# Kernel optimization log

Measured on AMD Instinct MI355X. Metric: run time of the kernel, lower is better.

## Reference

```python
import jax, jax.numpy as jnp
import numpy as np

EPS = 1e-5

def _layernorm(x, g, b):
    m = jnp.mean(x, axis=-1, keepdims=True)
    v = jnp.mean((x - m) ** 2, axis=-1, keepdims=True)
    return (x - m) * jax.lax.rsqrt(v + EPS) * g + b

def setup_inputs() -> dict:
    key = jax.random.key(0)
    ks = jax.random.split(key, 20)
    B, H, D = 8192, 50, 128
    NUM_USERS, NUM_NEWS, NUM_GNN = 200000, 100000, 80000
    s = 0.05
    user_table = jax.random.normal(ks[0], (NUM_USERS, D), jnp.float32) * s
    news_table = jax.random.normal(ks[1], (NUM_NEWS, D), jnp.float32) * s
    news_table = news_table.at[0].set(0.0)  # padding_idx=0
    inp = {
        "user_idx": jax.random.randint(ks[2], (B,), 0, NUM_USERS, jnp.int64 if jax.config.jax_enable_x64 else jnp.int32),
        "news_idx": jax.random.randint(ks[3], (B,), 0, NUM_NEWS, jnp.int32),
        "history": jax.random.randint(ks[4], (B, H), 0, NUM_NEWS, jnp.int32),
        "gnn_embeddings": jax.random.normal(ks[5], (NUM_GNN, D), jnp.float32) * s,
        "user_table": user_table,
        "news_table": news_table,
        "fusion_w": jax.random.normal(ks[6], (2 * D, D), jnp.float32) * s,
        "fusion_b": jnp.zeros((D,), jnp.float32),
        "ln_g": jnp.ones((D,), jnp.float32),
        "ln_b": jnp.zeros((D,), jnp.float32),
        "attn1_w": jax.random.normal(ks[7], (D, D // 2), jnp.float32) * s,
        "attn1_b": jnp.zeros((D // 2,), jnp.float32),
        "attn2_w": jax.random.normal(ks[8], (D // 2, 1), jnp.float32) * s,
        "attn2_b": jnp.zeros((1,), jnp.float32),
        "ut_w": jax.random.normal(ks[9], (D, D), jnp.float32) * s,
        "ut_b": jnp.zeros((D,), jnp.float32),
        "nt_w": jax.random.normal(ks[10], (D, D), jnp.float32) * s,
        "nt_b": jnp.zeros((D,), jnp.float32),
    }
    return inp

def reference(user_idx, news_idx, history, gnn_embeddings, user_table, news_table,
              fusion_w, fusion_b, ln_g, ln_b, attn1_w, attn1_b, attn2_w, attn2_b,
              ut_w, ut_b, nt_w, nt_b):
    num_gnn = gnn_embeddings.shape[0]

    def gather_gnn(idx):
        # masked gather: zeros where idx >= num_gnn
        valid = idx < num_gnn
        g = gnn_embeddings[jnp.clip(idx, 0, num_gnn - 1)]
        return jnp.where(valid[..., None], g, 0.0)

    def fusion(x):  # Linear(2D->D) + LayerNorm + ReLU (dropout=identity in eval)
        return jax.nn.relu(_layernorm(x @ fusion_w + fusion_b, ln_g, ln_b))

    # ---- user representation ----
    user_emb = user_table[user_idx]                       # (B, D)
    hist_id_emb = news_table[history]                     # (B, H, D)
    hist_gnn_emb = gather_gnn(history)                    # (B, H, D)
    hist_emb = fusion(jnp.concatenate([hist_id_emb, hist_gnn_emb], axis=-1))  # (B, H, D)
    mask = (history != 0)[..., None]                      # (B, H, 1)
    scores_h = jnp.tanh(hist_emb @ attn1_w + attn1_b) @ attn2_w + attn2_b      # (B, H, 1)
    scores_h = jnp.where(mask, scores_h, -1e9)
    attn = jax.nn.softmax(scores_h, axis=1)
    hist_repr = jnp.sum(hist_emb * attn, axis=1)          # (B, D)
    user_repr = jax.nn.relu((user_emb + hist_repr) @ ut_w + ut_b)

    # ---- news representation ----
    id_emb = news_table[news_idx]                         # (B, D)
    gnn_emb = gather_gnn(news_idx)
    fused = fusion(jnp.concatenate([id_emb, gnn_emb], axis=-1))
    news_repr = jax.nn.relu(fused @ nt_w + nt_b)

    return jax.nn.sigmoid(jnp.sum(user_repr * news_repr, axis=1))  # (B,)
```

## Files before the change

### kernel.cpp

```cpp
#include <hip/hip_runtime.h>
#include <math.h>

typedef __attribute__((ext_vector_type(8))) short bf16x8;
typedef __attribute__((ext_vector_type(4))) float f32x4;

#define TPB 256
#define HROWS 50
#define DDIM 128

static __device__ __forceinline__ unsigned short bf16_rne(float x) {
  union { float f; unsigned u; } v; v.f = x;
  return (unsigned short)((v.u + 0x7fffu + ((v.u >> 16) & 1u)) >> 16);
}
static __device__ __forceinline__ float bf16f(unsigned short h) {
  union { float f; unsigned u; } v; v.u = ((unsigned)h) << 16; return v.f;
}
static __device__ __forceinline__ void cvt_hilo(const float4 a, const float4 b,
                                                bf16x8& hi, bf16x8& lo) {
  unsigned short h;
  h = bf16_rne(a.x); hi[0] = (short)h; lo[0] = (short)bf16_rne(a.x - bf16f(h));
  h = bf16_rne(a.y); hi[1] = (short)h; lo[1] = (short)bf16_rne(a.y - bf16f(h));
  h = bf16_rne(a.z); hi[2] = (short)h; lo[2] = (short)bf16_rne(a.z - bf16f(h));
  h = bf16_rne(a.w); hi[3] = (short)h; lo[3] = (short)bf16_rne(a.w - bf16f(h));
  h = bf16_rne(b.x); hi[4] = (short)h; lo[4] = (short)bf16_rne(b.x - bf16f(h));
  h = bf16_rne(b.y); hi[5] = (short)h; lo[5] = (short)bf16_rne(b.y - bf16f(h));
  h = bf16_rne(b.z); hi[6] = (short)h; lo[6] = (short)bf16_rne(b.z - bf16f(h));
  h = bf16_rne(b.w); hi[7] = (short)h; lo[7] = (short)bf16_rne(b.w - bf16f(h));
}

#define WS_FWT_LO 32768
#define WS_A1T_HI 65536
#define WS_A1T_LO 73728

__global__ void prep_w(const float* __restrict__ fw, const float* __restrict__ a1w,
                       unsigned short* __restrict__ ws) {
  const int t = threadIdx.x, j = blockIdx.x;
  if (j < 128) {
    float x = fw[(size_t)t * 128 + j];
    unsigned short hi = bf16_rne(x);
    unsigned short lo = bf16_rne(x - bf16f(hi));
    ws[j * 256 + t] = hi;
    ws[WS_FWT_LO + j * 256 + t] = lo;
  } else if (t < 128) {
    int jj = j - 128;
    float x = a1w[(size_t)t * 64 + jj];
    unsigned short hi = bf16_rne(x);
    unsigned short lo = bf16_rne(x - bf16f(hi));
    ws[WS_A1T_HI + jj * 128 + t] = hi;
    ws[WS_A1T_LO + jj * 128 + t] = lo;
  }
}

__global__ __launch_bounds__(TPB, 3)
void gnnrec_mfma(const int* __restrict__ user_idx,
                 const int* __restrict__ news_idx,
                 const int* __restrict__ history,
                 const float* __restrict__ gnn, int NGNN,
                 const float* __restrict__ user_table,
                 const float* __restrict__ news_table,
                 const float* __restrict__ fusion_b,
                 const float* __restrict__ ln_g,
                 const float* __restrict__ ln_b,
                 const float* __restrict__ attn1_b,
                 const float* __restrict__ attn2_w,
                 const float* __restrict__ attn2_b,
                 const float* __restrict__ ut_w,
                 const float* __restrict__ ut_b,
                 const float* __restrict__ nt_w,
                 const float* __restrict__ nt_b,
                 const unsigned short* __restrict__ ws,
                 float* __restrict__ out)
{
  __shared__ short WtH[128][40];
  __shared__ short WtL[128][40];
  __shared__ float hist_s[51][132];
  __shared__ float scratch[1024 + 384];
  __shared__ int   idx_s[64];
  __shared__ float score_s[HROWS];

  const int b    = blockIdx.x;
  const int t    = threadIdx.x;
  const int lane = t & 63;
  const int w    = t >> 6;
  const int c15  = lane & 15;
  const int g    = lane >> 4;

  if (t < HROWS)        idx_s[t] = history[b * HROWS + t];
  else if (t == HROWS)  idx_s[t] = news_idx[b];
  else if (t < 64)      idx_s[t] = 0;
  const int uidx = user_idx[b];
  __syncthreads();

  const int arow = 16 * w + c15;
  const int aidx = idx_s[arow];
  const float* news_row = news_table + (size_t)aidx * DDIM;
  const bool   gnn_ok   = aidx < NGNN;
  const float* gnn_row  = gnn + (size_t)(gnn_ok ? aidx : 0) * DDIM;

  f32x4 acc[8];
#pragma unroll
  for (int ct = 0; ct < 8; ++ct) acc[ct] = (f32x4){0.f, 0.f, 0.f, 0.f};

  const int sc = t >> 1, ss = (t & 1) * 16;

  for (int kb = 0; kb < 8; ++kb) {
    {
      const unsigned short* ph = ws + sc * 256 + kb * 32 + ss;
      const unsigned short* pl = ph + WS_FWT_LO;
      bf16x8 h0 = *(const bf16x8*)(ph);
      bf16x8 h1 = *(const bf16x8*)(ph + 8);
      bf16x8 l0 = *(const bf16x8*)(pl);
      bf16x8 l1 = *(const bf16x8*)(pl + 8);
      *(bf16x8*)&WtH[sc][ss]     = h0;
      *(bf16x8*)&WtH[sc][ss + 8] = h1;
      *(bf16x8*)&WtL[sc][ss]     = l0;
      *(bf16x8*)&WtL[sc][ss + 8] = l1;
    }
    float4 x0 = make_float4(0.f, 0.f, 0.f, 0.f);
    float4 x1 = make_float4(0.f, 0.f, 0.f, 0.f);
    if (kb < 4) {
      const float* p = news_row + kb * 32 + g * 8;
      x0 = *(const float4*)(p);
      x1 = *(const float4*)(p + 4);
    } else if (gnn_ok) {
      const float* p = gnn_row + (kb - 4) * 32 + g * 8;
      x0 = *(const float4*)(p);
      x1 = *(const float4*)(p + 4);
    }
    bf16x8 aH, aL;
    cvt_hilo(x0, x1, aH, aL);
    __syncthreads();

#pragma unroll
    for (int ct = 0; ct < 8; ++ct) {
      bf16x8 bH = *(const bf16x8*)&WtH[16 * ct + c15][g * 8];
      bf16x8 bL = *(const bf16x8*)&WtL[16 * ct + c15][g * 8];
      acc[ct] = __builtin_amdgcn_mfma_f32_16x16x32_bf16(aH, bH, acc[ct], 0, 0, 0);
      acc[ct] = __builtin_amdgcn_mfma_f32_16x16x32_bf16(aH, bL, acc[ct], 0, 0, 0);
      acc[ct] = __builtin_amdgcn_mfma_f32_16x16x32_bf16(aL, bH, acc[ct], 0, 0, 0);
    }
    __syncthreads();
  }

  {
    float fbv[8], lgv[8], lbv[8];
#pragma unroll
    for (int ct = 0; ct < 8; ++ct) {
      fbv[ct] = fusion_b[16 * ct + c15];
      lgv[ct] = ln_g[16 * ct + c15];
      lbv[ct] = ln_b[16 * ct + c15];
    }
#pragma unroll
    for (int reg = 0; reg < 4; ++reg) {
      float y[8];
      float s = 0.f, sq = 0.f;
#pragma unroll
      for (int ct = 0; ct < 8; ++ct) {
        y[ct] = acc[ct][reg] + fbv[ct];
        s += y[ct];
        sq += y[ct] * y[ct];
      }
#pragma unroll
      for (int off = 1; off <= 8; off <<= 1) {
        s  += __shfl_xor(s,  off);
        sq += __shfl_xor(sq, off);
      }
      float mean = s * (1.f / 128.f);
      float var  = sq * (1.f / 128.f) - mean * mean;
      float inv  = 1.f / sqrtf(var + 1e-5f);
      int row = 16 * w + 4 * g + reg;
      if (row < 51) {
#pragma unroll
        for (int ct = 0; ct < 8; ++ct) {
          float r = fmaxf((y[ct] - mean) * inv * lgv[ct] + lbv[ct], 0.f);
          hist_s[row][16 * ct + c15] = r;
        }
      }
    }
  }
  __syncthreads();

  const unsigned short* a1T_hi = ws + WS_A1T_HI;
  const unsigned short* a1T_lo = ws + WS_A1T_LO;
  const int hrow = (16 * w + c15) < 51 ? (16 * w + c15) : 50;

  f32x4 acc2[4];
#pragma unroll
  for (int ct = 0; ct < 4; ++ct) acc2[ct] = (f32x4){0.f, 0.f, 0.f, 0.f};

#pragma unroll
  for (int ks = 0; ks < 4; ++ks) {
    float4 h0 = *(const float4*)&hist_s[hrow][ks * 32 + g * 8];
    float4 h1 = *(const float4*)&hist_s[hrow][ks * 32 + g * 8 + 4];
    bf16x8 aH, aL;
    cvt_hilo(h0, h1, aH, aL);
#pragma unroll
    for (int ct = 0; ct < 4; ++ct) {
      const int col = 16 * ct + c15;
      bf16x8 bH = *(const bf16x8*)(a1T_hi + col * 128 + ks * 32 + g * 8);
      bf16x8 bL = *(const bf16x8*)(a1T_lo + col * 128 + ks * 32 + g * 8);
      acc2[ct] = __builtin_amdgcn_mfma_f32_16x16x32_bf16(aH, bH, acc2[ct], 0, 0, 0);
      acc2[ct] = __builtin_amdgcn_mfma_f32_16x16x32_bf16(aH, bL, acc2[ct], 0, 0, 0);
      acc2[ct] = __builtin_amdgcn_mfma_f32_16x16x32_bf16(aL, bH, acc2[ct], 0, 0, 0);
    }
  }

  {
    float a1bv[4], a2wv[4];
#pragma unroll
    for (int ct = 0; ct < 4; ++ct) {
      a1bv[ct] = attn1_b[16 * ct + c15];
      a2wv[ct] = attn2_w[16 * ct + c15];
    }
    const float a2b = attn2_b[0];
#pragma unroll
    for (int reg = 0; reg < 4; ++reg) {
      float p = 0.f;
#pragma unroll
      for (int ct = 0; ct < 4; ++ct)
        p += tanhf(acc2[ct][reg] + a1bv[ct]) * a2wv[ct];
#pragma unroll
      for (int off = 1; off <= 8; off <<= 1) p += __shfl_xor(p, off);
      int row = 16 * w + 4 * g + reg;
      if (row < HROWS && c15 == 0)
        score_s[row] = (idx_s[row] != 0) ? (p + a2b) : -1e9f;
    }
  }
  __syncthreads();

  float mx = -3.0e38f;
  for (int r = 0; r < HROWS; ++r) mx = fmaxf(mx, score_s[r]);
  __syncthreads();
  if (t < HROWS) score_s[t] = __expf(score_s[t] - mx);
  __syncthreads();
  float denom = 0.f;
  for (int r = 0; r < HROWS; ++r) denom += score_s[r];
  const float invd = 1.f / denom;

  float* red = scratch;
  {
    int g8 = t >> 5, j4 = (t & 31) * 4;
    float p0 = 0.f, p1 = 0.f, p2 = 0.f, p3 = 0.f;
    for (int r = g8; r < HROWS; r += 8) {
      float wr = score_s[r] * invd;
      float4 hv = *(const float4*)&hist_s[r][j4];
      p0 = fmaf(wr, hv.x, p0);
      p1 = fmaf(wr, hv.y, p1);
      p2 = fmaf(wr, hv.z, p2);
      p3 = fmaf(wr, hv.w, p3);
    }
    *(float4*)&red[g8 * 128 + j4] = make_float4(p0, p1, p2, p3);
  }
  __syncthreads();

  float* u_s  = scratch + 1024;
  float* ur_s = scratch + 1152;
  float* nr_s = scratch + 1280;
  if (t < 128) {
    float hr = 0.f;
#pragma unroll
    for (int q = 0; q < 8; ++q) hr += red[q * 128 + t];
    u_s[t] = user_table[(size_t)uidx * DDIM + t] + hr;
  }
  __syncthreads();

  {
    int path = t >> 7, j = t & 127;
    const float* Wm  = path ? nt_w : ut_w;
    const float* bm  = path ? nt_b : ut_b;
    const float* src = path ? &hist_s[50][0] : u_s;
    float a = 0.f;
#pragma unroll 8
    for (int k4 = 0; k4 < 32; ++k4) {
      float4 sv = *(const float4*)&src[k4 * 4];
      a = fmaf(sv.x, Wm[(size_t)(k4 * 4 + 0) * 128 + j], a);
      a = fmaf(sv.y, Wm[(size_t)(k4 * 4 + 1) * 128 + j], a);
      a = fmaf(sv.z, Wm[(size_t)(k4 * 4 + 2) * 128 + j], a);
      a = fmaf(sv.w, Wm[(size_t)(k4 * 4 + 3) * 128 + j], a);
    }
    a = fmaxf(a + bm[j], 0.f);
    (path ? nr_s : ur_s)[j] = a;
  }
  __syncthreads();

  if (t < 64) {
    float p = ur_s[t] * nr_s[t] + ur_s[t + 64] * nr_s[t + 64];
    p += __shfl_xor(p, 1);
    p += __shfl_xor(p, 2);
    p += __shfl_xor(p, 4);
    p += __shfl_xor(p, 8);
    p += __shfl_xor(p, 16);
    p += __shfl_xor(p, 32);
    if (t == 0) out[b] = 1.f / (1.f + __expf(-p));
  }
}

extern "C" void kernel_launch(void* const* d_in, const int* in_sizes, int n_in,
                              void* d_out, int out_size, void* d_ws, size_t ws_size,
                              hipStream_t stream) {
  const int*   user_idx   = (const int*)d_in[0];
  const int*   news_idx   = (const int*)d_in[1];
  const int*   history    = (const int*)d_in[2];
  const float* gnn        = (const float*)d_in[3];
  const float* user_table = (const float*)d_in[4];
  const float* news_table = (const float*)d_in[5];
  const float* fusion_w   = (const float*)d_in[6];
  const float* fusion_b   = (const float*)d_in[7];
  const float* ln_g       = (const float*)d_in[8];
  const float* ln_b       = (const float*)d_in[9];
  const float* attn1_w    = (const float*)d_in[10];
  const float* attn1_b    = (const float*)d_in[11];
  const float* attn2_w    = (const float*)d_in[12];
  const float* attn2_b    = (const float*)d_in[13];
  const float* ut_w       = (const float*)d_in[14];
  const float* ut_b       = (const float*)d_in[15];
  const float* nt_w       = (const float*)d_in[16];
  const float* nt_b       = (const float*)d_in[17];

  const int B    = in_sizes[0];
  const int NGNN = in_sizes[3] / DDIM;
  float* out = (float*)d_out;
  unsigned short* ws = (unsigned short*)d_ws;

  prep_w<<<192, 256, 0, stream>>>(fusion_w, attn1_w, ws);

  gnnrec_mfma<<<B, TPB, 0, stream>>>(user_idx, news_idx, history, gnn, NGNN,
                                     user_table, news_table, fusion_b,
                                     ln_g, ln_b, attn1_b, attn2_w, attn2_b,
                                     ut_w, ut_b, nt_w, nt_b, ws, out);
}
```

Measured before the change: 549.8 us.

## Read fusion weights straight from global, prefetch gathers, fast tanh, tiled prep transpose

```diff
diff --git a/kernel.cpp b/kernel.cpp
--- a/kernel.cpp
+++ b/kernel.cpp
@@ -28,30 +28,47 @@
   h = bf16_rne(b.w); hi[7] = (short)h; lo[7] = (short)bf16_rne(b.w - bf16f(h));
 }
 
+static __device__ __forceinline__ float fast_tanh(float x) {
+  float xc = fminf(fmaxf(x, -15.f), 15.f);
+  float e  = __expf(2.f * xc);
+  return (e - 1.f) / (e + 1.f);
+}
+
 #define WS_FWT_LO 32768
 #define WS_A1T_HI 65536
 #define WS_A1T_LO 73728
 
 __global__ void prep_w(const float* __restrict__ fw, const float* __restrict__ a1w,
                        unsigned short* __restrict__ ws) {
-  const int t = threadIdx.x, j = blockIdx.x;
-  if (j < 128) {
-    float x = fw[(size_t)t * 128 + j];
+  __shared__ float tile[64][65];
+  const int bid = blockIdx.x, t = threadIdx.x;
+  const int ty = t >> 6, tx = t & 63;
+
+  const float* src; int W, K, ti, tj; unsigned short *dh, *dl;
+  if (bid < 8) { src = fw;  W = 128; K = 256; ti = bid >> 1; tj = bid & 1;
+                 dh = ws;             dl = ws + WS_FWT_LO; }
+  else         { src = a1w; W = 64;  K = 128; ti = bid - 8; tj = 0;
+                 dh = ws + WS_A1T_HI; dl = ws + WS_A1T_LO; }
+
+#pragma unroll
+  for (int rr = 0; rr < 16; ++rr) {
+    int r = ty * 16 + rr;
+    tile[r][tx] = src[(size_t)(ti * 64 + r) * W + tj * 64 + tx];
+  }
+  __syncthreads();
+#pragma unroll
+  for (int cc = 0; cc < 16; ++cc) {
+    int c = ty * 16 + cc;
+    float x = tile[tx][c];
     unsigned short hi = bf16_rne(x);
     unsigned short lo = bf16_rne(x - bf16f(hi));
-    ws[j * 256 + t] = hi;
-    ws[WS_FWT_LO + j * 256 + t] = lo;
-  } else if (t < 128) {
-    int jj = j - 128;
-    float x = a1w[(size_t)t * 64 + jj];
-    unsigned short hi = bf16_rne(x);
-    unsigned short lo = bf16_rne(x - bf16f(hi));
-    ws[WS_A1T_HI + jj * 128 + t] = hi;
-    ws[WS_A1T_LO + jj * 128 + t] = lo;
-  }
-}
-
-__global__ __launch_bounds__(TPB, 3)
+    size_t o = (size_t)(tj * 64 + c) * K + ti * 64 + tx;
+    dh[o] = hi;
+    dl[o] = lo;
+  }
+}
+
+__global__ __launch_bounds__(TPB, 4)
 void gnnrec_mfma(const int* __restrict__ user_idx,
                  const int* __restrict__ news_idx,
                  const int* __restrict__ history,
@@ -71,8 +88,6 @@
                  const unsigned short* __restrict__ ws,
                  float* __restrict__ out)
 {
-  __shared__ short WtH[128][40];
-  __shared__ short WtL[128][40];
   __shared__ float hist_s[51][132];
   __shared__ float scratch[1024 + 384];
   __shared__ int   idx_s[64];
@@ -101,45 +116,33 @@
 #pragma unroll
   for (int ct = 0; ct < 8; ++ct) acc[ct] = (f32x4){0.f, 0.f, 0.f, 0.f};
 
-  const int sc = t >> 1, ss = (t & 1) * 16;
+  float4 xc0 = *(const float4*)(news_row + g * 8);
+  float4 xc1 = *(const float4*)(news_row + g * 8 + 4);
 
   for (int kb = 0; kb < 8; ++kb) {
-    {
-      const unsigned short* ph = ws + sc * 256 + kb * 32 + ss;
-      const unsigned short* pl = ph + WS_FWT_LO;
-      bf16x8 h0 = *(const bf16x8*)(ph);
-      bf16x8 h1 = *(const bf16x8*)(ph + 8);
-      bf16x8 l0 = *(const bf16x8*)(pl);
-      bf16x8 l1 = *(const bf16x8*)(pl + 8);
-      *(bf16x8*)&WtH[sc][ss]     = h0;
-      *(bf16x8*)&WtH[sc][ss + 8] = h1;
-      *(bf16x8*)&WtL[sc][ss]     = l0;
-      *(bf16x8*)&WtL[sc][ss + 8] = l1;
-    }
-    float4 x0 = make_float4(0.f, 0.f, 0.f, 0.f);
-    float4 x1 = make_float4(0.f, 0.f, 0.f, 0.f);
-    if (kb < 4) {
-      const float* p = news_row + kb * 32 + g * 8;
-      x0 = *(const float4*)(p);
-      x1 = *(const float4*)(p + 4);
-    } else if (gnn_ok) {
-      const float* p = gnn_row + (kb - 4) * 32 + g * 8;
-      x0 = *(const float4*)(p);
-      x1 = *(const float4*)(p + 4);
+    float4 xn0 = make_float4(0.f, 0.f, 0.f, 0.f), xn1 = xn0;
+    if (kb < 7) {
+      int kn = kb + 1;
+      if (kn < 4) {
+        const float* p = news_row + kn * 32 + g * 8;
+        xn0 = *(const float4*)p; xn1 = *(const float4*)(p + 4);
+      } else if (gnn_ok) {
+        const float* p = gnn_row + (kn - 4) * 32 + g * 8;
+        xn0 = *(const float4*)p; xn1 = *(const float4*)(p + 4);
+      }
     }
     bf16x8 aH, aL;
-    cvt_hilo(x0, x1, aH, aL);
-    __syncthreads();
-
+    cvt_hilo(xc0, xc1, aH, aL);
 #pragma unroll
     for (int ct = 0; ct < 8; ++ct) {
-      bf16x8 bH = *(const bf16x8*)&WtH[16 * ct + c15][g * 8];
-      bf16x8 bL = *(const bf16x8*)&WtL[16 * ct + c15][g * 8];
+      const unsigned short* pH = ws + (16 * ct + c15) * 256 + kb * 32 + g * 8;
+      bf16x8 bH = *(const bf16x8*)pH;
+      bf16x8 bL = *(const bf16x8*)(pH + WS_FWT_LO);
       acc[ct] = __builtin_amdgcn_mfma_f32_16x16x32_bf16(aH, bH, acc[ct], 0, 0, 0);
       acc[ct] = __builtin_amdgcn_mfma_f32_16x16x32_bf16(aH, bL, acc[ct], 0, 0, 0);
       acc[ct] = __builtin_amdgcn_mfma_f32_16x16x32_bf16(aL, bH, acc[ct], 0, 0, 0);
     }
-    __syncthreads();
+    xc0 = xn0; xc1 = xn1;
   }
 
   {
@@ -181,27 +184,30 @@
   __syncthreads();
 
   const unsigned short* a1T_hi = ws + WS_A1T_HI;
-  const unsigned short* a1T_lo = ws + WS_A1T_LO;
   const int hrow = (16 * w + c15) < 51 ? (16 * w + c15) : 50;
 
-  f32x4 acc2[4];
-#pragma unroll
-  for (int ct = 0; ct < 4; ++ct) acc2[ct] = (f32x4){0.f, 0.f, 0.f, 0.f};
-
+  bf16x8 aH2[4], aL2[4];
 #pragma unroll
   for (int ks = 0; ks < 4; ++ks) {
     float4 h0 = *(const float4*)&hist_s[hrow][ks * 32 + g * 8];
     float4 h1 = *(const float4*)&hist_s[hrow][ks * 32 + g * 8 + 4];
-    bf16x8 aH, aL;
-    cvt_hilo(h0, h1, aH, aL);
-#pragma unroll
-    for (int ct = 0; ct < 4; ++ct) {
-      const int col = 16 * ct + c15;
-      bf16x8 bH = *(const bf16x8*)(a1T_hi + col * 128 + ks * 32 + g * 8);
-      bf16x8 bL = *(const bf16x8*)(a1T_lo + col * 128 + ks * 32 + g * 8);
-      acc2[ct] = __builtin_amdgcn_mfma_f32_16x16x32_bf16(aH, bH, acc2[ct], 0, 0, 0);
-      acc2[ct] = __builtin_amdgcn_mfma_f32_16x16x32_bf16(aH, bL, acc2[ct], 0, 0, 0);
-      acc2[ct] = __builtin_amdgcn_mfma_f32_16x16x32_bf16(aL, bH, acc2[ct], 0, 0, 0);
+    cvt_hilo(h0, h1, aH2[ks], aL2[ks]);
+  }
+
+  f32x4 acc2[4];
+#pragma unroll
+  for (int ct = 0; ct < 4; ++ct) acc2[ct] = (f32x4){0.f, 0.f, 0.f, 0.f};
+
+#pragma unroll
+  for (int ct = 0; ct < 4; ++ct) {
+    const unsigned short* pH = a1T_hi + (16 * ct + c15) * 128 + g * 8;
+#pragma unroll
+    for (int ks = 0; ks < 4; ++ks) {
+      bf16x8 bH = *(const bf16x8*)(pH + ks * 32);
+      bf16x8 bL = *(const bf16x8*)(pH + 8192 + ks * 32);
+      acc2[ct] = __builtin_amdgcn_mfma_f32_16x16x32_bf16(aH2[ks], bH, acc2[ct], 0, 0, 0);
+      acc2[ct] = __builtin_amdgcn_mfma_f32_16x16x32_bf16(aH2[ks], bL, acc2[ct], 0, 0, 0);
+      acc2[ct] = __builtin_amdgcn_mfma_f32_16x16x32_bf16(aL2[ks], bH, acc2[ct], 0, 0, 0);
     }
   }
 
@@ -218,7 +224,7 @@
       float p = 0.f;
 #pragma unroll
       for (int ct = 0; ct < 4; ++ct)
-        p += tanhf(acc2[ct][reg] + a1bv[ct]) * a2wv[ct];
+        p += fast_tanh(acc2[ct][reg] + a1bv[ct]) * a2wv[ct];
 #pragma unroll
       for (int off = 1; off <= 8; off <<= 1) p += __shfl_xor(p, off);
       int row = 16 * w + 4 * g + reg;
@@ -322,7 +328,7 @@
   float* out = (float*)d_out;
   unsigned short* ws = (unsigned short*)d_ws;
 
-  prep_w<<<192, 256, 0, stream>>>(fusion_w, attn1_w, ws);
+  prep_w<<<10, 256, 0, stream>>>(fusion_w, attn1_w, ws);
 
   gnnrec_mfma<<<B, TPB, 0, stream>>>(user_idx, news_idx, history, gnn, NGNN,
                                      user_table, news_table, fusion_b,
```

New measurement: 846.0 us. 53.9% more time.
